# Kernel optimization log

Hardware: AMD Instinct MI355X
Metric: run time of the kernel (lower is better)

## Reference

```python
import jax, jax.numpy as jnp
import numpy as np

GRID_SHAPE = (96, 96, 96)
GRID_LOWER = np.array([-1.2, -1.2, -1.2], dtype=np.float32)
GRID_STEPS = np.array([0.025, 0.025, 0.025], dtype=np.float32)
BIG = 1e10  # sentinel for cells outside an SDF's volume (min-combine ignores them)


def setup_inputs() -> dict:
    key = jax.random.key(0)
    k1, k2, k3, k4, k5 = jax.random.split(key, 5)
    M, S = 16, 64        # SDF library size, per-SDF resolution S^3
    B, N = 2, 8          # scenes, SDF instances per scene
    sdfs = jax.random.normal(k1, (M, S * S * S), dtype=jnp.float32)
    sdf_shapes = jnp.full((M, 3), S, dtype=jnp.int32)
    indices = jax.random.randint(k2, (B, N), 0, M, dtype=jnp.int32)
    trans = jax.random.uniform(k3, (B, N, 3), minval=-1.0, maxval=1.0)
    quat = jax.random.normal(k4, (B, N, 4))
    quat = quat / jnp.linalg.norm(quat, axis=-1, keepdims=True)
    sdf_poses = jnp.concatenate([trans, quat], axis=-1).astype(jnp.float32)
    sdf_widths = (0.02 * (1.0 + 0.2 * jax.random.uniform(k5, (B, N, 3)))).astype(jnp.float32)
    return {"sdfs": sdfs, "sdf_shapes": sdf_shapes, "indices": indices,
            "sdf_poses": sdf_poses, "sdf_widths": sdf_widths}


def _rotate_inv(q, v):
    # rotate v by the inverse (conjugate) of unit quaternion q = (x, y, z, w)
    u = -q[..., :3]
    w = q[..., 3:4]
    uv = jnp.cross(u, v)
    return v + 2.0 * jnp.cross(u, uv + w * v)


def reference(sdfs, sdf_shapes, indices, sdf_poses, sdf_widths):
    B, N = indices.shape
    GX, GY, GZ = GRID_SHAPE
    lower = jnp.asarray(GRID_LOWER)
    steps = jnp.asarray(GRID_STEPS)
    # world coordinates of grid cell centers: [GX, GY, GZ, 3]
    mesh = jnp.stack(jnp.meshgrid(jnp.arange(GX), jnp.arange(GY), jnp.arange(GZ),
                                  indexing='ij'), axis=-1).astype(jnp.float32)
    p = lower + (mesh + 0.5) * steps

    t = sdf_poses[..., :3]                                     # [B, N, 3]
    q = sdf_poses[..., 3:]
    q = q / jnp.linalg.norm(q, axis=-1, keepdims=True)         # [B, N, 4]

    # transform grid points into each SDF's local frame: [B, N, GX, GY, GZ, 3]
    d = p[None, None] - t[:, :, None, None, None, :]
    local = _rotate_inv(q[:, :, None, None, None, :], d)

    shp = sdf_shapes[indices]                                  # [B, N, 3] int
    shpf = shp.astype(local.dtype)[:, :, None, None, None, :]
    # continuous voxel coords, samples at cell centers
    g = local / sdf_widths[:, :, None, None, None, :] - 0.5
    inside = jnp.all((g >= 0.0) & (g <= shpf - 1.0), axis=-1)  # [B, N, GX, GY, GZ]
    f = jnp.clip(g, 0.0, shpf - 1.0)
    i0 = jnp.floor(f).astype(jnp.int32)
    frac = f - i0.astype(f.dtype)

    SX = shp[..., 0][:, :, None, None, None]
    SY = shp[..., 1][:, :, None, None, None]
    SZ = shp[..., 2][:, :, None, None, None]
    sdf_flat = sdfs[indices]                                   # [B, N, D]

    acc = jnp.zeros((B, N, GX, GY, GZ), dtype=sdfs.dtype)
    for dx in (0, 1):
        for dy in (0, 1):
            for dz in (0, 1):
                ii = jnp.minimum(i0[..., 0] + dx, SX - 1)
                jj = jnp.minimum(i0[..., 1] + dy, SY - 1)
                kk = jnp.minimum(i0[..., 2] + dz, SZ - 1)
                w = ((frac[..., 0] if dx else 1.0 - frac[..., 0]) *
                     (frac[..., 1] if dy else 1.0 - frac[..., 1]) *
                     (frac[..., 2] if dz else 1.0 - frac[..., 2]))
                flat = (ii * SY + jj) * SZ + kk
                vals = jnp.take_along_axis(sdf_flat, flat.reshape(B, N, -1),
                                           axis=2).reshape(B, N, GX, GY, GZ)
                acc = acc + w * vals

    per_sdf = jnp.where(inside, acc, BIG)
    return jnp.min(per_sdf, axis=1)                            # [B, GX, GY, GZ]
```

## Files before the change

### kernel.cpp

```cpp
#include <hip/hip_runtime.h>

#define GXD 96
#define GYD 96
#define GZD 96
#define PTS_PER_B (GXD * GYD * GZD)
#define BLOCKS_PER_B (PTS_PER_B / 256)
#define RECSZ 56
#define BIGF 1e10f
#define GLOWER -1.2f
#define GSTEP 0.025f
#define EPS_G 1e-2f

__device__ __forceinline__ void rot_inv(float qx, float qy, float qz, float qw,
                                        float dx, float dy, float dz,
                                        float& rx, float& ry, float& rz)
{
    float ux = -qx, uy = -qy, uz = -qz;
    float uvx = uy * dz - uz * dy;
    float uvy = uz * dx - ux * dz;
    float uvz = ux * dy - uy * dx;
    float t2x = uvx + qw * dx;
    float t2y = uvy + qw * dy;
    float t2z = uvz + qw * dz;
    rx = dx + 2.0f * (uy * t2z - uz * t2y);
    ry = dy + 2.0f * (uz * t2x - ux * t2z);
    rz = dz + 2.0f * (ux * t2y - uy * t2x);
}

__device__ __forceinline__ float next_up(float a) { return __uint_as_float(__float_as_uint(a) + 1u); }
__device__ __forceinline__ float next_dn(float a) { return __uint_as_float(__float_as_uint(a) - 1u); }

__device__ float exact_lo(float w, float t)
{
    float a = t * w;
    while (a / w < t)            a = next_up(a);
    while (next_dn(a) / w >= t)  a = next_dn(a);
    return a;
}

__device__ float exact_hi(float w, float L)
{
    float a = L * w;
    while (a / w > L)            a = next_dn(a);
    while (next_up(a) / w <= L)  a = next_up(a);
    return a;
}

__global__ void prep_v7(const int* __restrict__ shapes,
                        const int* __restrict__ indices,
                        const float* __restrict__ poses,
                        const float* __restrict__ widths,
                        float* __restrict__ rec,
                        int BN, int sdf_stride)
{
    int bn = blockIdx.x * blockDim.x + threadIdx.x;
    if (bn >= BN) return;
    int m = indices[bn];
    const float* pp = poses + (size_t)bn * 7;
    float tx = pp[0], ty = pp[1], tz = pp[2];
    float qx = pp[3], qy = pp[4], qz = pp[5], qw = pp[6];
    float nrm = sqrtf(qx * qx + qy * qy + qz * qz + qw * qw);
    qx = qx / nrm; qy = qy / nrm; qz = qz / nrm; qw = qw / nrm;

    float wx = widths[bn * 3 + 0], wy = widths[bn * 3 + 1], wz = widths[bn * 3 + 2];
    int SX = shapes[m * 3 + 0], SY = shapes[m * 3 + 1], SZ = shapes[m * 3 + 2];
    float mx = (float)(SX - 1), my = (float)(SY - 1), mz = (float)(SZ - 1);

    float Ax = exact_lo(wx, 0.5f), Ay = exact_lo(wy, 0.5f), Az = exact_lo(wz, 0.5f);
    float Bx = exact_hi(wx, mx + 0.5f), By = exact_hi(wy, my + 0.5f), Bz = exact_hi(wz, mz + 0.5f);

    float xx = qx * qx, yy = qy * qy, zz = qz * qz;
    float xy = qx * qy, xz = qx * qz, yz = qy * qz;
    float wqx = qw * qx, wqy = qw * qy, wqz = qw * qz;
    float R00 = 1.0f - 2.0f * (yy + zz), R01 = 2.0f * (xy - wqz), R02 = 2.0f * (xz + wqy);
    float R10 = 2.0f * (xy + wqz), R11 = 1.0f - 2.0f * (xx + zz), R12 = 2.0f * (yz - wqx);
    float R20 = 2.0f * (xz - wqy), R21 = 2.0f * (yz + wqx), R22 = 1.0f - 2.0f * (xx + yy);

    float cx = 0.5f * (Ax + Bx), cy = 0.5f * (Ay + By), cz = 0.5f * (Az + Bz);
    float hx = 0.5f * (Bx - Ax), hy = 0.5f * (By - Ay), hz = 0.5f * (Bz - Az);
    const float MARG = 2e-3f;
    float wcx = tx + R00 * cx + R01 * cy + R02 * cz;
    float wcy = ty + R10 * cx + R11 * cy + R12 * cz;
    float wcz = tz + R20 * cx + R21 * cy + R22 * cz;
    float ex = fabsf(R00) * hx + fabsf(R01) * hy + fabsf(R02) * hz + MARG;
    float ey = fabsf(R10) * hx + fabsf(R11) * hy + fabsf(R12) * hz + MARG;
    float ez = fabsf(R20) * hx + fabsf(R21) * hy + fabsf(R22) * hz + MARG;

    float iwx = 1.0f / wx, iwy = 1.0f / wy, iwz = 1.0f / wz;
    float Mg0x = iwx * R00, Mg1x = iwx * R10, Mg2x = iwx * R20;
    float Mg0y = iwy * R01, Mg1y = iwy * R11, Mg2y = iwy * R21;
    float Mg0z = iwz * R02, Mg1z = iwz * R12, Mg2z = iwz * R22;
    float Cgx = -0.5f - (Mg0x * tx + Mg1x * ty + Mg2x * tz);
    float Cgy = -0.5f - (Mg0y * tx + Mg1y * ty + Mg2y * tz);
    float Cgz = -0.5f - (Mg0z * tx + Mg1z * ty + Mg2z * tz);

    float* r = rec + (size_t)bn * RECSZ;
    r[0] = tx;  r[1] = ty;  r[2] = tz;
    r[3] = qx;  r[4] = qy;  r[5] = qz;  r[6] = qw;
    r[7] = iwx; r[8] = iwy; r[9] = iwz;
    r[10] = mx; r[11] = my; r[12] = mz;
    r[13] = Ax; r[14] = Ay; r[15] = Az;
    r[16] = Bx; r[17] = By; r[18] = Bz;
    int* ri = (int*)r;
    ri[19] = m * sdf_stride;
    ri[20] = SX; ri[21] = SY; ri[22] = SZ;
    r[23] = 0.0f;
    r[24] = wcx - ex; r[25] = wcy - ey; r[26] = wcz - ez;
    r[27] = wcx + ex; r[28] = wcy + ey; r[29] = wcz + ez;
    r[30] = 0.0f; r[31] = 0.0f;
    r[32] = Mg0x; r[33] = Mg1x; r[34] = Mg2x;
    r[35] = Mg0y; r[36] = Mg1y; r[37] = Mg2y;
    r[38] = Mg0z; r[39] = Mg1z; r[40] = Mg2z;
    r[41] = Cgx; r[42] = Cgy; r[43] = Cgz;
    r[44] = mx + EPS_G; r[45] = my + EPS_G; r[46] = mz + EPS_G;
    r[47] = 0.0f;
    r[48] = mx - EPS_G; r[49] = my - EPS_G; r[50] = mz - EPS_G;
    r[51] = 0.0f; r[52] = 0.0f; r[53] = 0.0f; r[54] = 0.0f; r[55] = 0.0f;
}

struct __attribute__((aligned(4))) F2 { float lo, hi; };

__device__ __forceinline__ float trilerp_g(const float* __restrict__ sd,
                                           float gx, float gy, float gz,
                                           float mx, float my, float mz,
                                           int SX, int SY, int SZ)
{
    float fx = fminf(fmaxf(gx, 0.0f), mx);
    float fy = fminf(fmaxf(gy, 0.0f), my);
    float fz = fminf(fmaxf(gz, 0.0f), mz);
    int i0x = (int)fx, i0y = (int)fy, i0z = (int)fz;
    float frx = fx - (float)i0x;
    float fry = fy - (float)i0y;
    float frz = fz - (float)i0z;
    int i1x = min(i0x + 1, SX - 1);
    int i1y = min(i0y + 1, SY - 1);

    int zb = min(i0z, max(SZ - 2, 0));
    bool at0 = (i0z == zb);

    int b00 = (i0x * SY + i0y) * SZ + zb;
    int b01 = (i0x * SY + i1y) * SZ + zb;
    int b10 = (i1x * SY + i0y) * SZ + zb;
    int b11 = (i1x * SY + i1y) * SZ + zb;

    F2 p00 = *(const F2*)(sd + b00);
    F2 p01 = *(const F2*)(sd + b01);
    F2 p10 = *(const F2*)(sd + b10);
    F2 p11 = *(const F2*)(sd + b11);

    float v000 = at0 ? p00.lo : p00.hi, v001 = p00.hi;
    float v010 = at0 ? p01.lo : p01.hi, v011 = p01.hi;
    float v100 = at0 ? p10.lo : p10.hi, v101 = p10.hi;
    float v110 = at0 ? p11.lo : p11.hi, v111 = p11.hi;

    float c00 = v000 + frz * (v001 - v000);
    float c01 = v010 + frz * (v011 - v010);
    float c10 = v100 + frz * (v101 - v100);
    float c11 = v110 + frz * (v111 - v110);
    float c0 = c00 + fry * (c01 - c00);
    float c1 = c10 + fry * (c11 - c10);
    return c0 + frx * (c1 - c0);
}

__global__ __launch_bounds__(256) void sdf_grid_v7(
    const float* __restrict__ sdfs,
    const float* __restrict__ rec,
    float* __restrict__ out,
    int N)
{
    int pid = blockIdx.x * blockDim.x + threadIdx.x;
    int b = blockIdx.y;

    int z = pid % GZD;
    int y = (pid / GZD) % GYD;
    int x = pid / (GZD * GYD);

    float px = GLOWER + ((float)x + 0.5f) * GSTEP;
    float py = GLOWER + ((float)y + 0.5f) * GSTEP;
    float pz = GLOWER + ((float)z + 0.5f) * GSTEP;

    size_t out_idx = (size_t)b * PTS_PER_B + pid;

    int pid0 = blockIdx.x * 256;
    int col0 = pid0 / GZD;
    int col2 = (pid0 + 255) / GZD;
    float bpx  = GLOWER + ((float)(col0 / GYD) + 0.5f) * GSTEP;
    float bpyl = GLOWER + ((float)(col0 % GYD) + 0.5f) * GSTEP;
    float bpyh = GLOWER + ((float)(col2 % GYD) + 0.5f) * GSTEP;
    float bpzl = GLOWER + 0.5f * GSTEP;
    float bpzh = GLOWER + ((float)(GZD - 1) + 0.5f) * GSTEP;

    int lane = threadIdx.x & 63;
    bool lok = false;
    if (lane < N) {
        const float* r = rec + (size_t)(b * N + lane) * RECSZ;
        lok = (bpx  >= r[24]) & (bpx  <= r[27]) &
              (bpyh >= r[25]) & (bpyl <= r[28]) &
              (bpzh >= r[26]) & (bpzl <= r[29]);
    }
    unsigned int msk = (unsigned int)__ballot(lok);

    if (msk == 0u) { out[out_idx] = BIGF; return; }

    float best = BIGF;

    for (int n = 0; n < N; ++n) {
        if (!((msk >> n) & 1u)) continue;

        const float* r = rec + (size_t)(b * N + n) * RECSZ;

        float sgx = fmaf(r[32], px, fmaf(r[33], py, fmaf(r[34], pz, r[41])));
        float sgy = fmaf(r[35], px, fmaf(r[36], py, fmaf(r[37], pz, r[42])));
        float sgz = fmaf(r[38], px, fmaf(r[39], py, fmaf(r[40], pz, r[43])));

        bool wide = (sgx >= -EPS_G) & (sgx <= r[44]) &
                    (sgy >= -EPS_G) & (sgy <= r[45]) &
                    (sgz >= -EPS_G) & (sgz <= r[46]);
        if (!wide) continue;

        bool narrow = (sgx >= EPS_G) & (sgx <= r[48]) &
                      (sgy >= EPS_G) & (sgy <= r[49]) &
                      (sgz >= EPS_G) & (sgz <= r[50]);

        float gx = sgx, gy = sgy, gz = sgz;
        bool inside = true;
        if (!narrow) {
            float dx = px - r[0], dy = py - r[1], dz = pz - r[2];
            float rx, ry, rz;
            rot_inv(r[3], r[4], r[5], r[6], dx, dy, dz, rx, ry, rz);
            inside = (rx >= r[13]) & (rx <= r[16]) &
                     (ry >= r[14]) & (ry <= r[17]) &
                     (rz >= r[15]) & (rz <= r[18]);
            gx = rx * r[7] - 0.5f;
            gy = ry * r[8] - 0.5f;
            gz = rz * r[9] - 0.5f;
        }
        if (inside) {
            const int* ri = (const int*)r;
            float v = trilerp_g(sdfs + ri[19], gx, gy, gz,
                                r[10], r[11], r[12],
                                ri[20], ri[21], ri[22]);
            best = fminf(best, v);
        }
    }

    out[out_idx] = best;
}

__global__ __launch_bounds__(256) void sdf_grid_kernel(
    const float* __restrict__ sdfs,
    const int*   __restrict__ sdf_shapes,
    const int*   __restrict__ indices,
    const float* __restrict__ poses,
    const float* __restrict__ widths,
    float*       __restrict__ out,
    int total, int N, int sdf_stride)
{
    int idx = blockIdx.x * blockDim.x + threadIdx.x;
    if (idx >= total) return;
    int z = idx % GZD;
    int y = (idx / GZD) % GYD;
    int x = (idx / (GZD * GYD)) % GXD;
    int b = idx / (GZD * GYD * GXD);
    float px = GLOWER + ((float)x + 0.5f) * GSTEP;
    float py = GLOWER + ((float)y + 0.5f) * GSTEP;
    float pz = GLOWER + ((float)z + 0.5f) * GSTEP;
    float best = BIGF;
    for (int n = 0; n < N; ++n) {
        int bn = b * N + n;
        int m  = indices[bn];
        const float* pp = poses + (size_t)bn * 7;
        float tx = pp[0], ty = pp[1], tz = pp[2];
        float qx = pp[3], qy = pp[4], qz = pp[5], qw = pp[6];
        float nrm = sqrtf(qx * qx + qy * qy + qz * qz + qw * qw);
        qx = qx / nrm; qy = qy / nrm; qz = qz / nrm; qw = qw / nrm;
        float dx = px - tx, dy = py - ty, dz = pz - tz;
        float rx, ry, rz;
        rot_inv(qx, qy, qz, qw, dx, dy, dz, rx, ry, rz);
        const float* ww = widths + (size_t)bn * 3;
        float gx = rx / ww[0] - 0.5f;
        float gy = ry / ww[1] - 0.5f;
        float gz = rz / ww[2] - 0.5f;
        int SX = sdf_shapes[m * 3 + 0];
        int SY = sdf_shapes[m * 3 + 1];
        int SZ = sdf_shapes[m * 3 + 2];
        float mx = (float)(SX - 1), my = (float)(SY - 1), mz = (float)(SZ - 1);
        bool inside = (gx >= 0.0f) && (gx <= mx) &&
                      (gy >= 0.0f) && (gy <= my) &&
                      (gz >= 0.0f) && (gz <= mz);
        float fx = fminf(fmaxf(gx, 0.0f), mx);
        float fy = fminf(fmaxf(gy, 0.0f), my);
        float fz = fminf(fmaxf(gz, 0.0f), mz);
        int i0x = (int)floorf(fx), i0y = (int)floorf(fy), i0z = (int)floorf(fz);
        float frx = fx - (float)i0x, fry = fy - (float)i0y, frz = fz - (float)i0z;
        int i1x = min(i0x + 1, SX - 1);
        int i1y = min(i0y + 1, SY - 1);
        int i1z = min(i0z + 1, SZ - 1);
        const float* sd = sdfs + (size_t)m * sdf_stride;
        int b00 = (i0x * SY + i0y) * SZ;
        int b01 = (i0x * SY + i1y) * SZ;
        int b10 = (i1x * SY + i0y) * SZ;
        int b11 = (i1x * SY + i1y) * SZ;
        float v000 = sd[b00 + i0z], v001 = sd[b00 + i1z];
        float v010 = sd[b01 + i0z], v011 = sd[b01 + i1z];
        float v100 = sd[b10 + i0z], v101 = sd[b10 + i1z];
        float v110 = sd[b11 + i0z], v111 = sd[b11 + i1z];
        float wx0 = 1.0f - frx, wx1 = frx;
        float wy0 = 1.0f - fry, wy1 = fry;
        float wz0 = 1.0f - frz, wz1 = frz;
        float acc = wx0 * wy0 * wz0 * v000 + wx0 * wy0 * wz1 * v001
                  + wx0 * wy1 * wz0 * v010 + wx0 * wy1 * wz1 * v011
                  + wx1 * wy0 * wz0 * v100 + wx1 * wy0 * wz1 * v101
                  + wx1 * wy1 * wz0 * v110 + wx1 * wy1 * wz1 * v111;
        float val = inside ? acc : BIGF;
        best = fminf(best, val);
    }
    out[idx] = best;
}

extern "C" void kernel_launch(void* const* d_in, const int* in_sizes, int n_in,
                              void* d_out, int out_size, void* d_ws, size_t ws_size,
                              hipStream_t stream) {
    const float* sdfs    = (const float*)d_in[0];
    const int*   shapes  = (const int*)d_in[1];
    const int*   indices = (const int*)d_in[2];
    const float* poses   = (const float*)d_in[3];
    const float* widths  = (const float*)d_in[4];
    float*       out     = (float*)d_out;

    int M = in_sizes[1] / 3;
    int sdf_stride = in_sizes[0] / M;
    int B = out_size / PTS_PER_B;
    int N = in_sizes[2] / B;
    int BN = B * N;

    size_t ws_needed = (size_t)BN * RECSZ * sizeof(float);

    if (ws_size >= ws_needed && N <= 32 && (PTS_PER_B % 256) == 0) {
        float* rec = (float*)d_ws;
        prep_v7<<<(BN + 63) / 64, 64, 0, stream>>>(
            shapes, indices, poses, widths, rec, BN, sdf_stride);
        dim3 grid(BLOCKS_PER_B, B);
        sdf_grid_v7<<<grid, 256, 0, stream>>>(sdfs, rec, out, N);
    } else {
        int total = out_size;
        int blocks = (total + 255) / 256;
        sdf_grid_kernel<<<blocks, 256, 0, stream>>>(
            sdfs, shapes, indices, poses, widths, out, total, N, sdf_stride);
    }
}
```

Baseline: 27.30 us.

## Map thread blocks to compact 3D bricks for tighter SDF culling

Each 256-thread block now covers an 8x8x4 brick of grid cells, and each wavefront covers a 4x4x4 sub-brick, instead of a linear run of cells along z. The per-block bounding box used in the ballot test against each SDF's AABB becomes much smaller, so more blocks can skip SDF instances or write the sentinel directly. Threads in a wave also sample nearby local coordinates, which may improve cache locality for the trilinear gathers. The cost is that output stores are no longer fully contiguous per wave, since only runs of 4 z-cells are adjacent, which hurts write coalescing.

```diff
diff --git a/kernel.cpp b/kernel.cpp
--- a/kernel.cpp
+++ b/kernel.cpp
@@ -4,7 +4,13 @@
 #define GYD 96
 #define GZD 96
 #define PTS_PER_B (GXD * GYD * GZD)
-#define BLOCKS_PER_B (PTS_PER_B / 256)
+#define BXC 8
+#define BYC 8
+#define BZC 4
+#define GXB (GXD / BXC)
+#define GYB (GYD / BYC)
+#define GZB (GZD / BZC)
+#define BLOCKS_PER_B (GXB * GYB * GZB)
 #define RECSZ 56
 #define BIGF 1e10f
 #define GLOWER -1.2f
@@ -46,7 +52,7 @@
     return a;
 }
 
-__global__ void prep_v7(const int* __restrict__ shapes,
+__global__ void prep_v8(const int* __restrict__ shapes,
                         const int* __restrict__ indices,
                         const float* __restrict__ poses,
                         const float* __restrict__ widths,
@@ -162,41 +168,49 @@
     return c0 + frx * (c1 - c0);
 }
 
-__global__ __launch_bounds__(256) void sdf_grid_v7(
+__global__ __launch_bounds__(256) void sdf_grid_v8(
     const float* __restrict__ sdfs,
     const float* __restrict__ rec,
     float* __restrict__ out,
     int N)
 {
-    int pid = blockIdx.x * blockDim.x + threadIdx.x;
+    int bidx = blockIdx.x;
     int b = blockIdx.y;
-
-    int z = pid % GZD;
-    int y = (pid / GZD) % GYD;
-    int x = pid / (GZD * GYD);
-
-    float px = GLOWER + ((float)x + 0.5f) * GSTEP;
-    float py = GLOWER + ((float)y + 0.5f) * GSTEP;
-    float pz = GLOWER + ((float)z + 0.5f) * GSTEP;
-
-    size_t out_idx = (size_t)b * PTS_PER_B + pid;
-
-    int pid0 = blockIdx.x * 256;
-    int col0 = pid0 / GZD;
-    int col2 = (pid0 + 255) / GZD;
-    float bpx  = GLOWER + ((float)(col0 / GYD) + 0.5f) * GSTEP;
-    float bpyl = GLOWER + ((float)(col0 % GYD) + 0.5f) * GSTEP;
-    float bpyh = GLOWER + ((float)(col2 % GYD) + 0.5f) * GSTEP;
-    float bpzl = GLOWER + 0.5f * GSTEP;
-    float bpzh = GLOWER + ((float)(GZD - 1) + 0.5f) * GSTEP;
-
-    int lane = threadIdx.x & 63;
+    int zb = bidx % GZB;
+    int yb = (bidx / GZB) % GYB;
+    int xb = bidx / (GZB * GYB);
+
+    int t = threadIdx.x;
+    int lane = t & 63;
+    int lz = lane & 3;
+    int ly = (lane >> 2) & 3;
+    int lx = lane >> 4;
+    int wx = (t >> 6) & 1;
+    int wy = t >> 7;
+
+    int cx = xb * BXC + wx * 4 + lx;
+    int cy = yb * BYC + wy * 4 + ly;
+    int cz = zb * BZC + lz;
+
+    float px = GLOWER + ((float)cx + 0.5f) * GSTEP;
+    float py = GLOWER + ((float)cy + 0.5f) * GSTEP;
+    float pz = GLOWER + ((float)cz + 0.5f) * GSTEP;
+
+    size_t out_idx = (size_t)b * PTS_PER_B + ((size_t)cx * GYD + cy) * GZD + cz;
+
+    float bxl = GLOWER + ((float)(xb * BXC) + 0.5f) * GSTEP;
+    float bxh = GLOWER + ((float)(xb * BXC + BXC - 1) + 0.5f) * GSTEP;
+    float byl = GLOWER + ((float)(yb * BYC) + 0.5f) * GSTEP;
+    float byh = GLOWER + ((float)(yb * BYC + BYC - 1) + 0.5f) * GSTEP;
+    float bzl = GLOWER + ((float)(zb * BZC) + 0.5f) * GSTEP;
+    float bzh = GLOWER + ((float)(zb * BZC + BZC - 1) + 0.5f) * GSTEP;
+
     bool lok = false;
     if (lane < N) {
         const float* r = rec + (size_t)(b * N + lane) * RECSZ;
-        lok = (bpx  >= r[24]) & (bpx  <= r[27]) &
-              (bpyh >= r[25]) & (bpyl <= r[28]) &
-              (bpzh >= r[26]) & (bpzl <= r[29]);
+        lok = (bxh >= r[24]) & (bxl <= r[27]) &
+              (byh >= r[25]) & (byl <= r[28]) &
+              (bzh >= r[26]) & (bzl <= r[29]);
     }
     unsigned int msk = (unsigned int)__ballot(lok);
 
@@ -338,10 +352,10 @@
 
     if (ws_size >= ws_needed && N <= 32 && (PTS_PER_B % 256) == 0) {
         float* rec = (float*)d_ws;
-        prep_v7<<<(BN + 63) / 64, 64, 0, stream>>>(
+        prep_v8<<<(BN + 63) / 64, 64, 0, stream>>>(
             shapes, indices, poses, widths, rec, BN, sdf_stride);
         dim3 grid(BLOCKS_PER_B, B);
-        sdf_grid_v7<<<grid, 256, 0, stream>>>(sdfs, rec, out, N);
+        sdf_grid_v8<<<grid, 256, 0, stream>>>(sdfs, rec, out, N);
     } else {
         int total = out_size;
         int blocks = (total + 255) / 256;
```

Result: faster. 25.95 us (-4.9%).
